# Kernel optimization log

Measured on AMD Instinct MI355X. Metric: run time of the kernel, lower is better.

## Reference

```python
import jax, jax.numpy as jnp
import numpy as np

DIM = 1024
N_HEADS = 16
HEAD_DIM = DIM // N_HEADS


def setup_inputs() -> dict:
    key = jax.random.key(0)
    k_x, k_wqkv, k_bqkv, k_wp, k_bp = jax.random.split(key, 5)
    s = 1.0 / np.sqrt(DIM)
    return {
        "x": jax.random.normal(k_x, (2, 2048, DIM), dtype=jnp.float32),
        "w_qkv": jax.random.uniform(k_wqkv, (3 * DIM, DIM), minval=-s, maxval=s, dtype=jnp.float32),
        "b_qkv": jax.random.uniform(k_bqkv, (3 * DIM,), minval=-s, maxval=s, dtype=jnp.float32),
        "w_proj": jax.random.uniform(k_wp, (DIM, DIM), minval=-s, maxval=s, dtype=jnp.float32),
        "b_proj": jax.random.uniform(k_bp, (DIM,), minval=-s, maxval=s, dtype=jnp.float32),
    }


def reference(x, w_qkv, b_qkv, w_proj, b_proj):
    B, S, D = x.shape
    H, Hd = N_HEADS, HEAD_DIM
    scale = jnp.asarray(Hd, x.dtype) ** 0.5
    qkv = x @ w_qkv.T + b_qkv                      # [B, S, 3D]
    q, k, v = jnp.split(qkv, 3, axis=-1)
    # [B, S, D] -> [B, H, S, Hd]
    q = q.reshape(B, S, H, Hd).transpose(0, 2, 1, 3)
    k = k.reshape(B, S, H, Hd).transpose(0, 2, 1, 3)
    v = v.reshape(B, S, H, Hd).transpose(0, 2, 1, 3)
    attn = jnp.einsum("bhqd,bhkd->bhqk", q, k) / scale
    attn = jax.nn.softmax(attn, axis=-1)
    out = jnp.einsum("bhqk,bhkd->bhqd", attn, v)   # [B, H, S, Hd]
    out = out.transpose(0, 2, 1, 3).reshape(B, S, D)
    return out @ w_proj.T + b_proj
```

## Files before the change

### kernel.cpp

```cpp
#include <hip/hip_runtime.h>

typedef __bf16 bf16;
typedef __bf16 bf16x4 __attribute__((ext_vector_type(4)));
typedef __bf16 bf16x8 __attribute__((ext_vector_type(8)));
typedef float f32x4 __attribute__((ext_vector_type(4)));
typedef float f32x16 __attribute__((ext_vector_type(16)));

#define DIMD 1024
#define NHEAD 16
#define HDIM 64
#define BATCH 2
#define SEQ 2048
#define MTOT (BATCH*SEQ)

#define EXP2F(x) __builtin_amdgcn_exp2f(x)

#define OFF_VT    (0ull)
#define OFF_WQKV  (8ull<<20)
#define OFF_OB    (8ull<<20)
#define OFF_WPROJ (0ull)

__device__ __forceinline__ void g2l16(const void* g, void* l) {
  __builtin_amdgcn_global_load_lds(
      (const __attribute__((address_space(1))) void*)g,
      (__attribute__((address_space(3))) void*)l,
      16, 0, 0);
}

__global__ __launch_bounds__(256) void cvt_kernel(const float* __restrict__ in,
                                                  bf16* __restrict__ out, int n4) {
  int i = blockIdx.x * blockDim.x + threadIdx.x;
  if (i < n4) {
    float4 v = ((const float4*)in)[i];
    bf16x4 o = { (bf16)v.x, (bf16)v.y, (bf16)v.z, (bf16)v.w };
    ((bf16x4*)out)[i] = o;
  }
}

__global__ __launch_bounds__(256, 2) void gemm_qkv(
    const float* __restrict__ x, const bf16* __restrict__ Wt,
    const float* __restrict__ bias,
    bf16* __restrict__ Qb, bf16* __restrict__ Kb, bf16* __restrict__ Vt)
{
  __shared__ bf16 lA[128 * 32];
  __shared__ bf16 lB[128 * 32];
  const int tid = threadIdx.x;
  const int wave = tid >> 6, lane = tid & 63;
  const int l15 = lane & 15, quad = lane >> 4;
  const int wm = wave >> 1, wn = wave & 1;
  const int tm = blockIdx.y * 128, tn = blockIdx.x * 128;

  f32x4 acc[4][4] = {};

  const int arowA = tid >> 1;
  const int acolA = (tid & 1) * 16;
  const int brow = tid >> 2;
  const int bchunk = (tid & 3) * 8;

  for (int kb = 0; kb < DIMD; kb += 32) {
    const float* gx = &x[(size_t)(tm + arowA) * DIMD + kb + acolA];
    float4 v0 = ((const float4*)gx)[0];
    float4 v1 = ((const float4*)gx)[1];
    float4 v2 = ((const float4*)gx)[2];
    float4 v3 = ((const float4*)gx)[3];
    __syncthreads();
    const bf16* gB = &Wt[(size_t)(tn + brow) * DIMD + kb + bchunk];
    g2l16(gB,                     &lB[wave * 512]);
    g2l16(gB + (size_t)64 * DIMD, &lB[2048 + wave * 512]);
    bf16x8 a0 = { (bf16)v0.x, (bf16)v0.y, (bf16)v0.z, (bf16)v0.w,
                  (bf16)v1.x, (bf16)v1.y, (bf16)v1.z, (bf16)v1.w };
    bf16x8 a1 = { (bf16)v2.x, (bf16)v2.y, (bf16)v2.z, (bf16)v2.w,
                  (bf16)v3.x, (bf16)v3.y, (bf16)v3.z, (bf16)v3.w };
    *(bf16x8*)&lA[arowA * 32 + acolA]     = a0;
    *(bf16x8*)&lA[arowA * 32 + acolA + 8] = a1;
    __syncthreads();

    bf16x8 af[4], bfr[4];
#pragma unroll
    for (int i = 0; i < 4; i++)
      af[i] = *(const bf16x8*)&lA[(wm * 64 + i * 16 + l15) * 32 + quad * 8];
#pragma unroll
    for (int i = 0; i < 4; i++)
      bfr[i] = *(const bf16x8*)&lB[(wn * 64 + i * 16 + l15) * 32 + quad * 8];
#pragma unroll
    for (int i = 0; i < 4; i++)
#pragma unroll
      for (int j = 0; j < 4; j++)
        acc[i][j] = __builtin_amdgcn_mfma_f32_16x16x32_bf16(af[i], bfr[j], acc[i][j], 0, 0, 0);
  }

  const int sel = tn >> 10;
#pragma unroll
  for (int j = 0; j < 4; j++) {
    const int n = tn + wn * 64 + j * 16 + l15;
    const float bv = bias[n];
    const int d = n & 1023, h = d >> 6, hd = d & 63;
#pragma unroll
    for (int i = 0; i < 4; i++) {
      const int mbase = tm + wm * 64 + i * 16 + quad * 4;
      const int b = mbase >> 11, s0 = mbase & 2047;
      const int bh = b * NHEAD + h;
      if (sel == 2) {
        bf16x4 vv = { (bf16)(acc[i][j][0] + bv), (bf16)(acc[i][j][1] + bv),
                      (bf16)(acc[i][j][2] + bv), (bf16)(acc[i][j][3] + bv) };
        *(bf16x4*)&Vt[((size_t)bh * HDIM + hd) * SEQ + s0] = vv;
      } else {
#pragma unroll
        for (int r = 0; r < 4; r++) {
          float v = acc[i][j][r] + bv;
          if (sel == 0)
            Qb[((size_t)bh * SEQ + s0 + r) * HDIM + hd] = (bf16)(v * 0.18033688f);
          else
            Kb[((size_t)bh * SEQ + s0 + r) * HDIM + hd] = (bf16)v;
        }
      }
    }
  }
}

__global__ __launch_bounds__(256, 2) void gemm_proj(
    const bf16* __restrict__ A, const bf16* __restrict__ Bt,
    const float* __restrict__ bias, float* __restrict__ out)
{
  __shared__ bf16 lA[64 * 32];
  __shared__ bf16 lB[128 * 32];
  const int tid = threadIdx.x;
  const int wave = tid >> 6, lane = tid & 63;
  const int l15 = lane & 15, quad = lane >> 4;
  const int tm = blockIdx.y * 64, tn = blockIdx.x * 128;

  f32x4 acc[4][2] = {};
  const int row = tid >> 2;
  const int ch = (tid & 3) * 8;

  for (int kb = 0; kb < DIMD; kb += 32) {
    __syncthreads();
    g2l16(&A[(size_t)(tm + row) * DIMD + kb + ch],        &lA[wave * 512]);
    g2l16(&Bt[(size_t)(tn + row) * DIMD + kb + ch],       &lB[wave * 512]);
    g2l16(&Bt[(size_t)(tn + 64 + row) * DIMD + kb + ch],  &lB[2048 + wave * 512]);
    __syncthreads();

    bf16x8 af[4], bfr[2];
#pragma unroll
    for (int i = 0; i < 4; i++)
      af[i] = *(const bf16x8*)&lA[(i * 16 + l15) * 32 + quad * 8];
#pragma unroll
    for (int j = 0; j < 2; j++)
      bfr[j] = *(const bf16x8*)&lB[(wave * 32 + j * 16 + l15) * 32 + quad * 8];
#pragma unroll
    for (int i = 0; i < 4; i++)
#pragma unroll
      for (int j = 0; j < 2; j++)
        acc[i][j] = __builtin_amdgcn_mfma_f32_16x16x32_bf16(af[i], bfr[j], acc[i][j], 0, 0, 0);
  }

#pragma unroll
  for (int j = 0; j < 2; j++) {
    const int n = tn + wave * 32 + j * 16 + l15;
    const float bv = bias[n];
#pragma unroll
    for (int i = 0; i < 4; i++) {
      const int mbase = tm + i * 16 + quad * 4;
#pragma unroll
      for (int r = 0; r < 4; r++)
        out[(size_t)(mbase + r) * DIMD + n] = acc[i][j][r] + bv;
    }
  }
}

#define LSTR 72
__global__ __launch_bounds__(256, 2) void attn_kernel(
    const bf16* __restrict__ Qb, const bf16* __restrict__ Kb,
    const bf16* __restrict__ Vt, bf16* __restrict__ Ob)
{
  __shared__ bf16 lKV[2][2][64 * LSTR];
  __shared__ bf16 lP[4][32 * LSTR];

  const int tid = threadIdx.x;
  const int wave = tid >> 6, lane = tid & 63;
  const int l31 = lane & 31, h = lane >> 5;
  const int xcd = blockIdx.x & 7, grp = blockIdx.x >> 3;
  const int bh = xcd + 8 * (grp & 3);
  const int qt = grp >> 2;

  const int qrow = qt * 128 + wave * 32 + l31;
  const bf16* qp = Qb + ((size_t)bh * SEQ + qrow) * HDIM + h * 8;
  bf16x8 qf[4];
#pragma unroll
  for (int c = 0; c < 4; c++) qf[c] = *(const bf16x8*)(qp + c * 16);

  const int srow = tid >> 3;
  const int sch = (tid & 7) * 8;
  const bf16* kg = Kb + ((size_t)bh * SEQ + srow) * HDIM + sch;
  const bf16* vg = Vt + ((size_t)bh * HDIM + srow) * SEQ + sch;

  uint4 kr0 = *(const uint4*)(kg);
  uint4 kr1 = *(const uint4*)(kg + 32 * HDIM);
  uint4 vr0 = *(const uint4*)(vg);
  uint4 vr1 = *(const uint4*)(vg + 32 * SEQ);

  f32x16 o0 = {}, o1 = {};
  float mrow = -1e30f, lrow = 0.f;

  for (int kt = 0; kt < SEQ / 64; kt++) {
    bf16* sK = lKV[kt & 1][0];
    bf16* sV = lKV[kt & 1][1];
    *(uint4*)&sK[srow * LSTR + sch]        = kr0;
    *(uint4*)&sK[(32 + srow) * LSTR + sch] = kr1;
    *(uint4*)&sV[srow * LSTR + sch]        = vr0;
    *(uint4*)&sV[(32 + srow) * LSTR + sch] = vr1;
    __syncthreads();

    const int ktn = (kt + 1) & (SEQ / 64 - 1);
    kr0 = *(const uint4*)(kg + (size_t)ktn * 64 * HDIM);
    kr1 = *(const uint4*)(kg + (size_t)ktn * 64 * HDIM + 32 * HDIM);
    vr0 = *(const uint4*)(vg + ktn * 64);
    vr1 = *(const uint4*)(vg + ktn * 64 + 32 * SEQ);

    f32x16 s0 = {}, s1 = {};
#pragma unroll
    for (int c = 0; c < 4; c++) {
      bf16x8 k0 = *(const bf16x8*)&sK[l31 * LSTR + c * 16 + h * 8];
      bf16x8 k1 = *(const bf16x8*)&sK[(32 + l31) * LSTR + c * 16 + h * 8];
      s0 = __builtin_amdgcn_mfma_f32_32x32x16_bf16(k0, qf[c], s0, 0, 0, 0);
      s1 = __builtin_amdgcn_mfma_f32_32x32x16_bf16(k1, qf[c], s1, 0, 0, 0);
    }

    float mx = -1e30f;
#pragma unroll
    for (int r = 0; r < 16; r++) { mx = fmaxf(mx, s0[r]); mx = fmaxf(mx, s1[r]); }
    mx = fmaxf(mx, __shfl_xor(mx, 32, 64));
    const float nm = fmaxf(mrow, mx);
    const float alpha = EXP2F(mrow - nm);
    mrow = nm;

    float rs = 0.f;
#pragma unroll
    for (int r = 0; r < 16; r++) {
      const float p0 = EXP2F(s0[r] - nm);
      const float p1 = EXP2F(s1[r] - nm);
      s0[r] = p0; s1[r] = p1;
      rs += p0 + p1;
    }
    rs += __shfl_xor(rs, 32, 64);
    lrow = lrow * alpha + rs;
#pragma unroll
    for (int r = 0; r < 16; r++) { o0[r] *= alpha; o1[r] *= alpha; }

#pragma unroll
    for (int g = 0; g < 4; g++) {
      bf16x4 pa = { (bf16)s0[4*g], (bf16)s0[4*g+1], (bf16)s0[4*g+2], (bf16)s0[4*g+3] };
      bf16x4 pb = { (bf16)s1[4*g], (bf16)s1[4*g+1], (bf16)s1[4*g+2], (bf16)s1[4*g+3] };
      *(bf16x4*)&lP[wave][l31 * LSTR + g * 8 + h * 4]      = pa;
      *(bf16x4*)&lP[wave][l31 * LSTR + 32 + g * 8 + h * 4] = pb;
    }
    bf16x8 pf[4];
#pragma unroll
    for (int c = 0; c < 4; c++)
      pf[c] = *(const bf16x8*)&lP[wave][l31 * LSTR + c * 16 + h * 8];

#pragma unroll
    for (int c = 0; c < 4; c++) {
      bf16x8 v0 = *(const bf16x8*)&sV[l31 * LSTR + c * 16 + h * 8];
      bf16x8 v1 = *(const bf16x8*)&sV[(32 + l31) * LSTR + c * 16 + h * 8];
      o0 = __builtin_amdgcn_mfma_f32_32x32x16_bf16(v0, pf[c], o0, 0, 0, 0);
      o1 = __builtin_amdgcn_mfma_f32_32x32x16_bf16(v1, pf[c], o1, 0, 0, 0);
    }
  }

  const int b = bh >> 4, head = bh & 15;
  const float inv = 1.f / lrow;
  const size_t base = ((size_t)b * SEQ + qrow) * DIMD + head * HDIM;
#pragma unroll
  for (int g = 0; g < 4; g++) {
    bf16x4 oa = { (bf16)(o0[4*g] * inv), (bf16)(o0[4*g+1] * inv),
                  (bf16)(o0[4*g+2] * inv), (bf16)(o0[4*g+3] * inv) };
    bf16x4 ob = { (bf16)(o1[4*g] * inv), (bf16)(o1[4*g+1] * inv),
                  (bf16)(o1[4*g+2] * inv), (bf16)(o1[4*g+3] * inv) };
    *(bf16x4*)&Ob[base + g * 8 + h * 4]      = oa;
    *(bf16x4*)&Ob[base + 32 + g * 8 + h * 4] = ob;
  }
}

extern "C" void kernel_launch(void* const* d_in, const int* in_sizes, int n_in,
                              void* d_out, int out_size, void* d_ws, size_t ws_size,
                              hipStream_t stream) {
  const float* x      = (const float*)d_in[0];
  const float* w_qkv  = (const float*)d_in[1];
  const float* b_qkv  = (const float*)d_in[2];
  const float* w_proj = (const float*)d_in[3];
  const float* b_proj = (const float*)d_in[4];
  float* out = (float*)d_out;
  char* ws = (char*)d_ws;

  bf16* Qb = (bf16*)d_out;
  bf16* Kb = (bf16*)d_out + (size_t)MTOT * DIMD;
  bf16* Vt     = (bf16*)(ws + OFF_VT);
  bf16* wqkvb  = (bf16*)(ws + OFF_WQKV);
  bf16* Ob     = (bf16*)(ws + OFF_OB);
  bf16* wprojb = (bf16*)(ws + OFF_WPROJ);

  cvt_kernel<<<(3 * DIMD * DIMD / 4) / 256, 256, 0, stream>>>(w_qkv, wqkvb, 3 * DIMD * DIMD / 4);
  gemm_qkv<<<dim3(24, 32), 256, 0, stream>>>(x, wqkvb, b_qkv, Qb, Kb, Vt);
  attn_kernel<<<BATCH * NHEAD * (SEQ / 128), 256, 0, stream>>>(Qb, Kb, Vt, Ob);
  cvt_kernel<<<(DIMD * DIMD / 4) / 256, 256, 0, stream>>>(w_proj, wprojb, DIMD * DIMD / 4);
  gemm_proj<<<dim3(8, 64), 256, 0, stream>>>(Ob, wprojb, b_proj, out);
}
```

Measured before the change: 204.9 us.

## Fuse weight fp32-to-bf16 conversion into GEMMs and double-buffer LDS with register prefetch

Removes the two separate weight conversion kernels; the QKV and projection GEMMs now read fp32 weights directly and convert to bf16 while staging into LDS. Both GEMMs gain double-buffered shared memory, with the next K tile prefetched into registers during the MFMA work, which drops one barrier per iteration. This saves two launches and a round trip of the weights through memory. In exchange, each block re-reads and re-converts fp32 weights (twice the bytes of bf16) and holds more registers and LDS.

```diff
diff --git a/kernel.cpp b/kernel.cpp
--- a/kernel.cpp
+++ b/kernel.cpp
@@ -15,35 +15,22 @@
 
 #define EXP2F(x) __builtin_amdgcn_exp2f(x)
 
-#define OFF_VT    (0ull)
-#define OFF_WQKV  (8ull<<20)
-#define OFF_OB    (8ull<<20)
-#define OFF_WPROJ (0ull)
-
-__device__ __forceinline__ void g2l16(const void* g, void* l) {
-  __builtin_amdgcn_global_load_lds(
-      (const __attribute__((address_space(1))) void*)g,
-      (__attribute__((address_space(3))) void*)l,
-      16, 0, 0);
-}
-
-__global__ __launch_bounds__(256) void cvt_kernel(const float* __restrict__ in,
-                                                  bf16* __restrict__ out, int n4) {
-  int i = blockIdx.x * blockDim.x + threadIdx.x;
-  if (i < n4) {
-    float4 v = ((const float4*)in)[i];
-    bf16x4 o = { (bf16)v.x, (bf16)v.y, (bf16)v.z, (bf16)v.w };
-    ((bf16x4*)out)[i] = o;
-  }
+#define OFF_VT (0ull)
+#define OFF_OB (8ull<<20)
+
+__device__ __forceinline__ bf16x8 cvt8(float4 a, float4 b) {
+  bf16x8 r = { (bf16)a.x, (bf16)a.y, (bf16)a.z, (bf16)a.w,
+               (bf16)b.x, (bf16)b.y, (bf16)b.z, (bf16)b.w };
+  return r;
 }
 
 __global__ __launch_bounds__(256, 2) void gemm_qkv(
-    const float* __restrict__ x, const bf16* __restrict__ Wt,
+    const float* __restrict__ x, const float* __restrict__ W,
     const float* __restrict__ bias,
     bf16* __restrict__ Qb, bf16* __restrict__ Kb, bf16* __restrict__ Vt)
 {
-  __shared__ bf16 lA[128 * 32];
-  __shared__ bf16 lB[128 * 32];
+  __shared__ bf16 lA[2][128 * 32];
+  __shared__ bf16 lB[2][128 * 32];
   const int tid = threadIdx.x;
   const int wave = tid >> 6, lane = tid & 63;
   const int l15 = lane & 15, quad = lane >> 4;
@@ -52,36 +39,38 @@
 
   f32x4 acc[4][4] = {};
 
-  const int arowA = tid >> 1;
-  const int acolA = (tid & 1) * 16;
-  const int brow = tid >> 2;
-  const int bchunk = (tid & 3) * 8;
-
-  for (int kb = 0; kb < DIMD; kb += 32) {
-    const float* gx = &x[(size_t)(tm + arowA) * DIMD + kb + acolA];
-    float4 v0 = ((const float4*)gx)[0];
-    float4 v1 = ((const float4*)gx)[1];
-    float4 v2 = ((const float4*)gx)[2];
-    float4 v3 = ((const float4*)gx)[3];
+  const int arow = tid >> 1, ahalf = (tid & 1) * 16;
+  const int brow = tid & 127, bhalf = (tid >> 7) * 16;
+  const float* ga = &x[(size_t)(tm + arow) * DIMD + ahalf];
+  const float* gb = &W[(size_t)(tn + brow) * DIMD + bhalf];
+
+  float4 av0 = ((const float4*)ga)[0], av1 = ((const float4*)ga)[1];
+  float4 av2 = ((const float4*)ga)[2], av3 = ((const float4*)ga)[3];
+  float4 bv0 = ((const float4*)gb)[0], bv1 = ((const float4*)gb)[1];
+  float4 bv2 = ((const float4*)gb)[2], bv3 = ((const float4*)gb)[3];
+
+  for (int kt = 0; kt < 32; kt++) {
+    bf16* sA = lA[kt & 1];
+    bf16* sB = lB[kt & 1];
+    *(bf16x8*)&sA[arow * 32 + ahalf]     = cvt8(av0, av1);
+    *(bf16x8*)&sA[arow * 32 + ahalf + 8] = cvt8(av2, av3);
+    *(bf16x8*)&sB[brow * 32 + bhalf]     = cvt8(bv0, bv1);
+    *(bf16x8*)&sB[brow * 32 + bhalf + 8] = cvt8(bv2, bv3);
     __syncthreads();
-    const bf16* gB = &Wt[(size_t)(tn + brow) * DIMD + kb + bchunk];
-    g2l16(gB,                     &lB[wave * 512]);
-    g2l16(gB + (size_t)64 * DIMD, &lB[2048 + wave * 512]);
-    bf16x8 a0 = { (bf16)v0.x, (bf16)v0.y, (bf16)v0.z, (bf16)v0.w,
-                  (bf16)v1.x, (bf16)v1.y, (bf16)v1.z, (bf16)v1.w };
-    bf16x8 a1 = { (bf16)v2.x, (bf16)v2.y, (bf16)v2.z, (bf16)v2.w,
-                  (bf16)v3.x, (bf16)v3.y, (bf16)v3.z, (bf16)v3.w };
-    *(bf16x8*)&lA[arowA * 32 + acolA]     = a0;
-    *(bf16x8*)&lA[arowA * 32 + acolA + 8] = a1;
-    __syncthreads();
+
+    const int kn = ((kt + 1) & 31) * 32;
+    const float4* gan = (const float4*)(ga + kn);
+    const float4* gbn = (const float4*)(gb + kn);
+    av0 = gan[0]; av1 = gan[1]; av2 = gan[2]; av3 = gan[3];
+    bv0 = gbn[0]; bv1 = gbn[1]; bv2 = gbn[2]; bv3 = gbn[3];
 
     bf16x8 af[4], bfr[4];
 #pragma unroll
     for (int i = 0; i < 4; i++)
-      af[i] = *(const bf16x8*)&lA[(wm * 64 + i * 16 + l15) * 32 + quad * 8];
-#pragma unroll
-    for (int i = 0; i < 4; i++)
-      bfr[i] = *(const bf16x8*)&lB[(wn * 64 + i * 16 + l15) * 32 + quad * 8];
+      af[i] = *(const bf16x8*)&sA[(wm * 64 + i * 16 + l15) * 32 + quad * 8];
+#pragma unroll
+    for (int i = 0; i < 4; i++)
+      bfr[i] = *(const bf16x8*)&sB[(wn * 64 + i * 16 + l15) * 32 + quad * 8];
 #pragma unroll
     for (int i = 0; i < 4; i++)
 #pragma unroll
@@ -119,34 +108,47 @@
 }
 
 __global__ __launch_bounds__(256, 2) void gemm_proj(
-    const bf16* __restrict__ A, const bf16* __restrict__ Bt,
+    const bf16* __restrict__ A, const float* __restrict__ W,
     const float* __restrict__ bias, float* __restrict__ out)
 {
-  __shared__ bf16 lA[64 * 32];
-  __shared__ bf16 lB[128 * 32];
+  __shared__ bf16 lA[2][64 * 32];
+  __shared__ bf16 lB[2][128 * 32];
   const int tid = threadIdx.x;
   const int wave = tid >> 6, lane = tid & 63;
   const int l15 = lane & 15, quad = lane >> 4;
   const int tm = blockIdx.y * 64, tn = blockIdx.x * 128;
 
   f32x4 acc[4][2] = {};
-  const int row = tid >> 2;
-  const int ch = (tid & 3) * 8;
-
-  for (int kb = 0; kb < DIMD; kb += 32) {
+
+  const int arow = tid >> 2, ach = (tid & 3) * 8;
+  const int brow = tid & 127, bhalf = (tid >> 7) * 16;
+  const bf16* ga = &A[(size_t)(tm + arow) * DIMD + ach];
+  const float* gb = &W[(size_t)(tn + brow) * DIMD + bhalf];
+
+  uint4 ar = *(const uint4*)ga;
+  float4 bv0 = ((const float4*)gb)[0], bv1 = ((const float4*)gb)[1];
+  float4 bv2 = ((const float4*)gb)[2], bv3 = ((const float4*)gb)[3];
+
+  for (int kt = 0; kt < 32; kt++) {
+    bf16* sA = lA[kt & 1];
+    bf16* sB = lB[kt & 1];
+    *(uint4*)&sA[arow * 32 + ach]        = ar;
+    *(bf16x8*)&sB[brow * 32 + bhalf]     = cvt8(bv0, bv1);
+    *(bf16x8*)&sB[brow * 32 + bhalf + 8] = cvt8(bv2, bv3);
     __syncthreads();
-    g2l16(&A[(size_t)(tm + row) * DIMD + kb + ch],        &lA[wave * 512]);
-    g2l16(&Bt[(size_t)(tn + row) * DIMD + kb + ch],       &lB[wave * 512]);
-    g2l16(&Bt[(size_t)(tn + 64 + row) * DIMD + kb + ch],  &lB[2048 + wave * 512]);
-    __syncthreads();
+
+    const int kn = ((kt + 1) & 31) * 32;
+    ar = *(const uint4*)(ga + kn);
+    const float4* gbn = (const float4*)(gb + kn);
+    bv0 = gbn[0]; bv1 = gbn[1]; bv2 = gbn[2]; bv3 = gbn[3];
 
     bf16x8 af[4], bfr[2];
 #pragma unroll
     for (int i = 0; i < 4; i++)
-      af[i] = *(const bf16x8*)&lA[(i * 16 + l15) * 32 + quad * 8];
+      af[i] = *(const bf16x8*)&sA[(i * 16 + l15) * 32 + quad * 8];
 #pragma unroll
     for (int j = 0; j < 2; j++)
-      bfr[j] = *(const bf16x8*)&lB[(wave * 32 + j * 16 + l15) * 32 + quad * 8];
+      bfr[j] = *(const bf16x8*)&sB[(wave * 32 + j * 16 + l15) * 32 + quad * 8];
 #pragma unroll
     for (int i = 0; i < 4; i++)
 #pragma unroll
@@ -295,14 +297,10 @@
 
   bf16* Qb = (bf16*)d_out;
   bf16* Kb = (bf16*)d_out + (size_t)MTOT * DIMD;
-  bf16* Vt     = (bf16*)(ws + OFF_VT);
-  bf16* wqkvb  = (bf16*)(ws + OFF_WQKV);
-  bf16* Ob     = (bf16*)(ws + OFF_OB);
-  bf16* wprojb = (bf16*)(ws + OFF_WPROJ);
-
-  cvt_kernel<<<(3 * DIMD * DIMD / 4) / 256, 256, 0, stream>>>(w_qkv, wqkvb, 3 * DIMD * DIMD / 4);
-  gemm_qkv<<<dim3(24, 32), 256, 0, stream>>>(x, wqkvb, b_qkv, Qb, Kb, Vt);
+  bf16* Vt = (bf16*)(ws + OFF_VT);
+  bf16* Ob = (bf16*)(ws + OFF_OB);
+
+  gemm_qkv<<<dim3(24, 32), 256, 0, stream>>>(x, w_qkv, b_qkv, Qb, Kb, Vt);
   attn_kernel<<<BATCH * NHEAD * (SEQ / 128), 256, 0, stream>>>(Qb, Kb, Vt, Ob);
-  cvt_kernel<<<(DIMD * DIMD / 4) / 256, 256, 0, stream>>>(w_proj, wprojb, DIMD * DIMD / 4);
-  gemm_proj<<<dim3(8, 64), 256, 0, stream>>>(Ob, wprojb, b_proj, out);
-}
+  gemm_proj<<<dim3(8, 64), 256, 0, stream>>>(Ob, w_proj, b_proj, out);
+}
```

New measurement: 244.5 us. 19.4% more time.
